# Optimization experiments

Measured on AMD Instinct MI355X. Metric: run time of the kernel, lower is better.

The kernel has to match this reference:

```python
import jax, jax.numpy as jnp
import numpy as np

RES = (128, 128, 128, 100)  # x, y, z, t resolutions
FEAT = 64
N = 1048576
HID = 64
COMBOS4 = [(0, 1), (0, 2), (0, 3), (1, 2), (1, 3), (2, 3)]  # temporal k-planes
COMBOS3 = [(0, 1), (0, 2), (1, 2)]  # spatial triplane


def setup_inputs() -> dict:
    key = jax.random.key(0)
    ks = jax.random.split(key, 16)
    d = {}
    d["inp"] = jax.random.uniform(ks[0], (N, 4), dtype=jnp.float32)  # xyz in [0,1], t in [0,1]
    d["aabb"] = jnp.array([[0.0, 0.0, 0.0], [1.0, 1.0, 1.0]], dtype=jnp.float32)
    # plane coefs: [feat, res[b], res[a]] per combo (a,b), uniform(init_a, init_b)
    for i, (a, b) in enumerate(COMBOS4):
        d[f"tp{i}"] = jax.random.uniform(ks[1 + i], (FEAT, RES[b], RES[a]),
                                         minval=0.1, maxval=0.5, dtype=jnp.float32)
    for i, (a, b) in enumerate(COMBOS3):
        d[f"sp{i}"] = jax.random.uniform(ks[7 + i], (FEAT, RES[b], RES[a]),
                                         minval=0.1, maxval=0.5, dtype=jnp.float32)
    in_dim = 2 * FEAT  # temporal + spatial features concatenated
    d["w0"] = (jax.random.normal(ks[10], (in_dim, HID), dtype=jnp.float32) / np.sqrt(in_dim)).astype(jnp.float32)
    d["b0"] = jnp.zeros((HID,), dtype=jnp.float32)
    d["w1"] = (jax.random.normal(ks[11], (HID, 3), dtype=jnp.float32) / np.sqrt(HID)).astype(jnp.float32)
    d["b1"] = jnp.zeros((3,), dtype=jnp.float32)
    return d


def _sample_plane(plane, cx, cy):
    """Bilinear grid_sample, align_corners=True. plane: [F,H,W]; cx,cy: [N] in [-1,1]. Returns [N,F]."""
    F_, H, W = plane.shape
    x = (cx + 1.0) * 0.5 * (W - 1)
    y = (cy + 1.0) * 0.5 * (H - 1)
    x0 = jnp.clip(jnp.floor(x).astype(jnp.int32), 0, W - 2)
    y0 = jnp.clip(jnp.floor(y).astype(jnp.int32), 0, H - 2)
    wx = (x - x0)[:, None]
    wy = (y - y0)[:, None]
    p = jnp.transpose(plane, (1, 2, 0))  # [H,W,F]
    v00 = p[y0, x0]
    v01 = p[y0, x0 + 1]
    v10 = p[y0 + 1, x0]
    v11 = p[y0 + 1, x0 + 1]
    return (v00 * (1 - wx) + v01 * wx) * (1 - wy) + (v10 * (1 - wx) + v11 * wx) * wy


def reference(inp, aabb, tp0, tp1, tp2, tp3, tp4, tp5, sp0, sp1, sp2, w0, b0, w1, b1):
    # normalize positions to [-1,1]
    pos = (inp[:, :3] - aabb[0]) / (aabb[1] - aabb[0]) * 2.0 - 1.0
    t = inp[:, 3:] * 2.0 - 1.0
    c = jnp.concatenate([pos, t], axis=-1)  # [N,4]
    tps = [tp0, tp1, tp2, tp3, tp4, tp5]
    feat_t = sum(_sample_plane(tps[i], c[:, a], c[:, b]) for i, (a, b) in enumerate(COMBOS4))
    sps = [sp0, sp1, sp2]
    feat_s = sum(_sample_plane(sps[i], pos[:, a], pos[:, b]) for i, (a, b) in enumerate(COMBOS3))
    feat = jnp.concatenate([feat_t, feat_s], axis=-1)  # [N, 2*FEAT]
    h = jax.nn.relu(feat @ w0 + b0)
    return h @ w1 + b1  # [N, 3]
```

## Files before the change

### kernel.cpp

```cpp
#include <hip/hip_runtime.h>
#include <hip/hip_fp16.h>

#define DEVFN __device__ __forceinline__

#if defined(__has_builtin)
#  if __has_builtin(__builtin_amdgcn_fdot2)
#    define HAS_FDOT2 1
#  endif
#endif

typedef _Float16 h2v __attribute__((ext_vector_type(2)));

struct PlanePtrs { const float* p[9]; };

__constant__ const int g_H[9] = {128,128,100,128,100,100,128,128,128};
__constant__ const int g_A[9] = {0,0,0,1,1,2,0,0,1};
__constant__ const int g_B[9] = {1,2,3,2,3,3,1,2,2};
__constant__ const int g_PRE[10] = {0,16384,32768,45568,61952,74752,87552,103936,120320,136704};
__constant__ const int g_OFF4[9] = {0,131072,262144,364544,495616,598016,700416,831488,962560};

static const int    TOTAL_TEXELS = 136704;
static const size_t WS_PLANES    = 17498112ull;
static const size_t WS_W0H       = 16384ull;
static const int    NBINS        = 2048;
static const int    NHB          = 256;

__global__ __launch_bounds__(256) void k_transpose(PlanePtrs ptrs, __half* __restrict__ dst)
{
    int gid = blockIdx.x * 256 + threadIdx.x;

    int pl = 0;
    #pragma unroll
    for (int i = 1; i < 9; ++i) if (gid >= g_PRE[i]) pl = i;
    int tx   = gid - g_PRE[pl];
    int nTex = g_PRE[pl + 1] - g_PRE[pl];

    const float* src = ptrs.p[0];
    #pragma unroll
    for (int i = 1; i < 9; ++i) if (pl == i) src = ptrs.p[i];
    src += tx;

    uint4* __restrict__ out4 = reinterpret_cast<uint4*>(dst) + (size_t)gid * 8;
    #pragma unroll
    for (int j = 0; j < 8; ++j) {
        float f0 = src[(8*j+0)*nTex];
        float f1 = src[(8*j+1)*nTex];
        float f2 = src[(8*j+2)*nTex];
        float f3 = src[(8*j+3)*nTex];
        float f4 = src[(8*j+4)*nTex];
        float f5 = src[(8*j+5)*nTex];
        float f6 = src[(8*j+6)*nTex];
        float f7 = src[(8*j+7)*nTex];
        uint4 u;
        u.x = __builtin_bit_cast(unsigned int, __floats2half2_rn(f0, f1));
        u.y = __builtin_bit_cast(unsigned int, __floats2half2_rn(f2, f3));
        u.z = __builtin_bit_cast(unsigned int, __floats2half2_rn(f4, f5));
        u.w = __builtin_bit_cast(unsigned int, __floats2half2_rn(f6, f7));
        out4[j] = u;
    }
}

__global__ __launch_bounds__(256) void k_w0pack(const float* __restrict__ w0,
                                                unsigned int* __restrict__ w0h)
{
    int idx = blockIdx.x * 256 + threadIdx.x;
    int d = idx >> 6, j = idx & 63;
    float a = w0[(2 * d) * 64 + j];
    float b = w0[(2 * d + 1) * 64 + j];
    w0h[idx] = __builtin_bit_cast(unsigned int, __floats2half2_rn(a, b));
}

DEVFN int point_key(float4 in, float a0x, float a0y, float a0z,
                    float isx, float isy, float isz)
{
    float x = (in.x - a0x) * isx;
    float y = (in.y - a0y) * isy;
    float z = (in.z - a0z) * isz;
    int xc = min(7, max(0, (int)(x * 8.0f)));
    int yc = min(7, max(0, (int)(y * 8.0f)));
    int zc = min(7, max(0, (int)(z * 8.0f)));
    int tc = min(3, max(0, (int)(in.w * 4.0f)));
    return (((xc << 3) | yc) << 3 | zc) << 2 | tc;
}

__global__ __launch_bounds__(256) void k_hist2(const float4* __restrict__ inp,
                                               const float* __restrict__ aabb,
                                               int N, int chunk,
                                               int* __restrict__ blkhist)
{
    __shared__ int hc[NBINS];
    const int tid = threadIdx.x, blk = blockIdx.x;
    #pragma unroll
    for (int j = 0; j < NBINS / 256; ++j) hc[tid + j * 256] = 0;
    __syncthreads();

    float a0x = aabb[0], a0y = aabb[1], a0z = aabb[2];
    float isx = 1.0f / (aabb[3] - a0x), isy = 1.0f / (aabb[4] - a0y), isz = 1.0f / (aabb[5] - a0z);

    int end = min(N, (blk + 1) * chunk);
    for (int i = blk * chunk + tid; i < end; i += 256)
        atomicAdd(&hc[point_key(inp[i], a0x, a0y, a0z, isx, isy, isz)], 1);

    __syncthreads();
    #pragma unroll
    for (int j = 0; j < NBINS / 256; ++j)
        blkhist[blk * NBINS + tid + j * 256] = hc[tid + j * 256];
}

__global__ __launch_bounds__(256) void k_scanA(int* __restrict__ blkhist,
                                               int* __restrict__ bintotal)
{
    int bin = blockIdx.x * 256 + threadIdx.x;
    int run = 0;
    for (int b = 0; b < NHB; ++b) {
        int v = blkhist[b * NBINS + bin];
        blkhist[b * NBINS + bin] = run;
        run += v;
    }
    bintotal[bin] = run;
}

__global__ __launch_bounds__(256) void k_scanB(const int* __restrict__ bintotal,
                                               int* __restrict__ binstart)
{
    int t = threadIdx.x;
    int v[8]; int sum = 0;
    #pragma unroll
    for (int j = 0; j < 8; ++j) { v[j] = bintotal[t * 8 + j]; sum += v[j]; }

    int lane = t & 63, w = t >> 6;
    int x = sum;
    #pragma unroll
    for (int d = 1; d < 64; d <<= 1) {
        int y = __shfl_up(x, d);
        if (lane >= d) x += y;
    }
    __shared__ int wsum[4];
    if (lane == 63) wsum[w] = x;
    __syncthreads();
    int woff = 0;
    for (int i = 0; i < w; ++i) woff += wsum[i];
    int run = woff + x - sum;
    #pragma unroll
    for (int j = 0; j < 8; ++j) { binstart[t * 8 + j] = run; run += v[j]; }
}

__global__ __launch_bounds__(256) void k_fill2(const float4* __restrict__ inp,
                                               const float* __restrict__ aabb,
                                               int N, int chunk,
                                               const int* __restrict__ blkhist,
                                               const int* __restrict__ binstart,
                                               int* __restrict__ order)
{
    __shared__ int hc[NBINS];
    const int tid = threadIdx.x, blk = blockIdx.x;
    #pragma unroll
    for (int j = 0; j < NBINS / 256; ++j) hc[tid + j * 256] = 0;
    __syncthreads();

    float a0x = aabb[0], a0y = aabb[1], a0z = aabb[2];
    float isx = 1.0f / (aabb[3] - a0x), isy = 1.0f / (aabb[4] - a0y), isz = 1.0f / (aabb[5] - a0z);

    int end = min(N, (blk + 1) * chunk);
    for (int i = blk * chunk + tid; i < end; i += 256) {
        int key = point_key(inp[i], a0x, a0y, a0z, isx, isy, isz);
        int lr  = atomicAdd(&hc[key], 1);
        order[binstart[key] + blkhist[blk * NBINS + key] + lr] = i;
    }
}

DEVFN void corner4f(unsigned a, unsigned b, unsigned c, unsigned d,
                    __half2 w00, __half2 w01, __half2 w10, __half2 w11,
                    float& ax, float& ay)
{
    __half2 t = __hmul2(__builtin_bit_cast(__half2, a), w00);
    t = __hfma2(__builtin_bit_cast(__half2, b), w01, t);
    t = __hfma2(__builtin_bit_cast(__half2, c), w10, t);
    t = __hfma2(__builtin_bit_cast(__half2, d), w11, t);
    ax += __low2float(t);
    ay += __high2float(t);
}

__global__ __launch_bounds__(64) void k_main(
    const float4* __restrict__ inp,
    const float*  __restrict__ aabb,
    const __half* __restrict__ planes,
    const unsigned int* __restrict__ w0h,
    const int*    __restrict__ order,
    int           useOrder,
    const float*  __restrict__ w0,
    const float*  __restrict__ b0,
    const float*  __restrict__ w1,
    const float*  __restrict__ b1,
    float*        __restrict__ out)
{
    __shared__ unsigned int lds[64 * 65];

    const int tid = threadIdx.x;
    const int g   = tid >> 3;
    const int k   = tid & 7;

    const int nwg = gridDim.x;
    const int bid = blockIdx.x;
    const int wid = ((nwg & 7) == 0) ? ((bid & 7) * (nwg >> 3) + (bid >> 3)) : bid;
    const int base = wid * 64;

    const int myord = useOrder ? order[base + tid] : (base + tid);

    float a0x = aabb[0], a0y = aabb[1], a0z = aabb[2];
    float sx  = aabb[3] - a0x, sy = aabb[4] - a0y, sz = aabb[5] - a0z;

    for (int q = 0; q < 8; ++q) {
        const int p = g * 8 + q;
        const int pidx = __shfl(myord, p);
        float4 in = inp[pidx];
        float c[4];
        c[0] = (in.x - a0x) / sx * 2.0f - 1.0f;
        c[1] = (in.y - a0y) / sy * 2.0f - 1.0f;
        c[2] = (in.z - a0z) / sz * 2.0f - 1.0f;
        c[3] = in.w * 2.0f - 1.0f;

        float accT[8], accS[8];
        #pragma unroll
        for (int j = 0; j < 8; ++j) { accT[j] = 0.0f; accS[j] = 0.0f; }

        #pragma unroll
        for (int pl = 0; pl < 9; ++pl) {
            const int W = 128;
            const int H = g_H[pl];
            float fx = (c[g_A[pl]] + 1.0f) * 0.5f * (float)(W - 1);
            float fy = (c[g_B[pl]] + 1.0f) * 0.5f * (float)(H - 1);
            int x0 = min(max((int)floorf(fx), 0), W - 2);
            int y0 = min(max((int)floorf(fy), 0), H - 2);
            float wx = fx - (float)x0;
            float wy = fy - (float)y0;
            float iwx = 1.0f - wx, iwy = 1.0f - wy;

            const uint4* pb = reinterpret_cast<const uint4*>(planes)
                            + g_OFF4[pl] + ((y0 << 7) + x0) * 8 + k;
            uint4 v00 = pb[0];
            uint4 v01 = pb[8];
            uint4 v10 = pb[1024];
            uint4 v11 = pb[1032];

            __half2 w00h = __float2half2_rn(iwx * iwy);
            __half2 w01h = __float2half2_rn(wx  * iwy);
            __half2 w10h = __float2half2_rn(iwx * wy);
            __half2 w11h = __float2half2_rn(wx  * wy);

            if (pl < 6) {
                corner4f(v00.x, v01.x, v10.x, v11.x, w00h, w01h, w10h, w11h, accT[0], accT[1]);
                corner4f(v00.y, v01.y, v10.y, v11.y, w00h, w01h, w10h, w11h, accT[2], accT[3]);
                corner4f(v00.z, v01.z, v10.z, v11.z, w00h, w01h, w10h, w11h, accT[4], accT[5]);
                corner4f(v00.w, v01.w, v10.w, v11.w, w00h, w01h, w10h, w11h, accT[6], accT[7]);
            } else {
                corner4f(v00.x, v01.x, v10.x, v11.x, w00h, w01h, w10h, w11h, accS[0], accS[1]);
                corner4f(v00.y, v01.y, v10.y, v11.y, w00h, w01h, w10h, w11h, accS[2], accS[3]);
                corner4f(v00.z, v01.z, v10.z, v11.z, w00h, w01h, w10h, w11h, accS[4], accS[5]);
                corner4f(v00.w, v01.w, v10.w, v11.w, w00h, w01h, w10h, w11h, accS[6], accS[7]);
            }
        }

        #pragma unroll
        for (int j = 0; j < 4; ++j) {
            lds[p * 65 +      k * 4 + j] =
                __builtin_bit_cast(unsigned int, __floats2half2_rn(accT[2*j], accT[2*j+1]));
            lds[p * 65 + 32 + k * 4 + j] =
                __builtin_bit_cast(unsigned int, __floats2half2_rn(accS[2*j], accS[2*j+1]));
        }
    }

    __syncthreads();

    const unsigned int* lrow = &lds[tid * 65];
    float o0 = b1[0], o1 = b1[1], o2 = b1[2];

    #pragma unroll 1
    for (int jc = 0; jc < 64; jc += 16) {
        float h[16];
        #pragma unroll
        for (int jj = 0; jj < 16; ++jj) h[jj] = b0[jc + jj];

        #pragma unroll 4
        for (int d = 0; d < 64; ++d) {
            unsigned u = lrow[d];
#if defined(HAS_FDOT2)
            h2v fv = __builtin_bit_cast(h2v, u);
            const unsigned int* wr = w0h + d * 64 + jc;
            #pragma unroll
            for (int jj = 0; jj < 16; ++jj)
                h[jj] = __builtin_amdgcn_fdot2(fv, __builtin_bit_cast(h2v, wr[jj]),
                                               h[jj], false);
#else
            __half2 hv = __builtin_bit_cast(__half2, u);
            float f0 = __low2float(hv);
            float f1 = __high2float(hv);
            const float* wr = w0 + d * 128 + jc;
            #pragma unroll
            for (int jj = 0; jj < 16; ++jj) h[jj] = fmaf(f0, wr[jj], h[jj]);
            #pragma unroll
            for (int jj = 0; jj < 16; ++jj) h[jj] = fmaf(f1, wr[64 + jj], h[jj]);
#endif
        }

        #pragma unroll
        for (int jj = 0; jj < 16; ++jj) {
            float r = fmaxf(h[jj], 0.0f);
            const float* wq = w1 + (jc + jj) * 3;
            o0 = fmaf(r, wq[0], o0);
            o1 = fmaf(r, wq[1], o1);
            o2 = fmaf(r, wq[2], o2);
        }
    }

    long long oo = (long long)myord * 3;
    out[oo + 0] = o0;
    out[oo + 1] = o1;
    out[oo + 2] = o2;
}

__global__ __launch_bounds__(256) void k_fallback(
    const float4* __restrict__ inp, const float* __restrict__ aabb, PlanePtrs ptrs,
    const float* __restrict__ w0, const float* __restrict__ b0,
    const float* __restrict__ w1, const float* __restrict__ b1,
    float* __restrict__ out, int N, int start)
{
    int pidx = start + blockIdx.x * 256 + threadIdx.x;
    if (pidx >= N) return;
    float4 in = inp[pidx];
    float c[4];
    c[0] = (in.x - aabb[0]) / (aabb[3] - aabb[0]) * 2.0f - 1.0f;
    c[1] = (in.y - aabb[1]) / (aabb[4] - aabb[1]) * 2.0f - 1.0f;
    c[2] = (in.z - aabb[2]) / (aabb[5] - aabb[2]) * 2.0f - 1.0f;
    c[3] = in.w * 2.0f - 1.0f;

    float h[64];
    #pragma unroll
    for (int j = 0; j < 64; ++j) h[j] = b0[j];

    #pragma unroll
    for (int pl = 0; pl < 9; ++pl) {
        const int W = 128, H = g_H[pl];
        float fx = (c[g_A[pl]] + 1.0f) * 0.5f * (float)(W - 1);
        float fy = (c[g_B[pl]] + 1.0f) * 0.5f * (float)(H - 1);
        int x0 = min(max((int)floorf(fx), 0), W - 2);
        int y0 = min(max((int)floorf(fy), 0), H - 2);
        float wx = fx - (float)x0, wy = fy - (float)y0;
        const float* P = ptrs.p[pl];
        int off = y0 * 128 + x0;
        int HW = H * 128;
        int row = (pl < 6) ? 0 : 64;
        for (int f = 0; f < 64; ++f) {
            const float* qp = P + f * HW + off;
            float v = (qp[0] * (1.0f - wx) + qp[1] * wx) * (1.0f - wy)
                    + (qp[128] * (1.0f - wx) + qp[129] * wx) * wy;
            const float* wr = w0 + (row + f) * 64;
            #pragma unroll
            for (int j = 0; j < 64; ++j) h[j] = fmaf(v, wr[j], h[j]);
        }
    }
    float o0 = b1[0], o1 = b1[1], o2 = b1[2];
    #pragma unroll
    for (int j = 0; j < 64; ++j) {
        float r = fmaxf(h[j], 0.0f);
        o0 = fmaf(r, w1[j * 3 + 0], o0);
        o1 = fmaf(r, w1[j * 3 + 1], o1);
        o2 = fmaf(r, w1[j * 3 + 2], o2);
    }
    out[(long long)pidx * 3 + 0] = o0;
    out[(long long)pidx * 3 + 1] = o1;
    out[(long long)pidx * 3 + 2] = o2;
}

extern "C" void kernel_launch(void* const* d_in, const int* in_sizes, int n_in,
                              void* d_out, int out_size, void* d_ws, size_t ws_size,
                              hipStream_t stream)
{
    const float4* inp  = (const float4*)d_in[0];
    const float*  aabb = (const float*)d_in[1];
    PlanePtrs ptrs;
    for (int i = 0; i < 9; ++i) ptrs.p[i] = (const float*)d_in[2 + i];
    const float* w0 = (const float*)d_in[11];
    const float* b0 = (const float*)d_in[12];
    const float* w1 = (const float*)d_in[13];
    const float* b1 = (const float*)d_in[14];
    float* out = (float*)d_out;
    const int N = in_sizes[0] / 4;

    const size_t off_w0h   = WS_PLANES;
    const size_t ws_base   = WS_PLANES + WS_W0H;
    const size_t off_order = ws_base;
    const size_t off_bh    = off_order + 4ull * (size_t)N;
    const size_t off_bt    = off_bh + (size_t)NHB * NBINS * 4;
    const size_t off_bs    = off_bt + NBINS * 4;
    const size_t need_sort = off_bs + NBINS * 4;

    if (ws_size >= ws_base && (N % 64) == 0) {
        __half* planes = (__half*)d_ws;
        unsigned int* w0h = (unsigned int*)((char*)d_ws + off_w0h);
        k_transpose<<<TOTAL_TEXELS / 256, 256, 0, stream>>>(ptrs, planes);
        k_w0pack<<<16, 256, 0, stream>>>(w0, w0h);

        if (ws_size >= need_sort) {
            int* order    = (int*)((char*)d_ws + off_order);
            int* blkhist  = (int*)((char*)d_ws + off_bh);
            int* bintotal = (int*)((char*)d_ws + off_bt);
            int* binstart = (int*)((char*)d_ws + off_bs);
            int chunk = (((N + NHB - 1) / NHB) + 255) / 256 * 256;

            k_hist2<<<NHB, 256, 0, stream>>>(inp, aabb, N, chunk, blkhist);
            k_scanA<<<NBINS / 256, 256, 0, stream>>>(blkhist, bintotal);
            k_scanB<<<1, 256, 0, stream>>>(bintotal, binstart);
            k_fill2<<<NHB, 256, 0, stream>>>(inp, aabb, N, chunk, blkhist, binstart, order);
            k_main<<<N / 64, 64, 0, stream>>>(inp, aabb, planes, w0h, order, 1,
                                              w0, b0, w1, b1, out);
        } else {
            k_main<<<N / 64, 64, 0, stream>>>(inp, aabb, planes, w0h, (const int*)nullptr, 0,
                                              w0, b0, w1, b1, out);
        }
    } else {
        k_fallback<<<(N + 255) / 256, 256, 0, stream>>>(inp, aabb, ptrs, w0, b0, w1, b1, out, N, 0);
    }
}
```

Baseline: 363.5 us.

## Software-pipeline plane gathers with 4-deep register ring and shuffle coords

Each lane now loads and normalizes its own input point once, and the coordinates are broadcast with shuffles instead of every lane re-reading inp through a shuffled index. All 9 plane offsets and bilinear weights are computed up front. Corner loads run through a 4-slot register ring so that up to four planes' gathers are in flight while earlier planes are accumulated. The outer q loop is marked unroll 1. This raises register pressure (64 VGPRs for the ring plus the weights) and may cut occupancy.

```diff
diff --git a/kernel.cpp b/kernel.cpp
--- a/kernel.cpp
+++ b/kernel.cpp
@@ -210,54 +210,85 @@
     float a0x = aabb[0], a0y = aabb[1], a0z = aabb[2];
     float sx  = aabb[3] - a0x, sy = aabb[4] - a0y, sz = aabb[5] - a0z;
 
+    float4 min_ = inp[myord];
+    float c0 = (min_.x - a0x) / sx * 2.0f - 1.0f;
+    float c1 = (min_.y - a0y) / sy * 2.0f - 1.0f;
+    float c2 = (min_.z - a0z) / sz * 2.0f - 1.0f;
+    float c3 = min_.w * 2.0f - 1.0f;
+
+    const uint4* pbase = reinterpret_cast<const uint4*>(planes);
+
+    #pragma unroll 1
     for (int q = 0; q < 8; ++q) {
         const int p = g * 8 + q;
-        const int pidx = __shfl(myord, p);
-        float4 in = inp[pidx];
-        float c[4];
-        c[0] = (in.x - a0x) / sx * 2.0f - 1.0f;
-        c[1] = (in.y - a0y) / sy * 2.0f - 1.0f;
-        c[2] = (in.z - a0z) / sz * 2.0f - 1.0f;
-        c[3] = in.w * 2.0f - 1.0f;
-
-        float accT[8], accS[8];
-        #pragma unroll
-        for (int j = 0; j < 8; ++j) { accT[j] = 0.0f; accS[j] = 0.0f; }
-
+        float cc[4];
+        cc[0] = __shfl(c0, p);
+        cc[1] = __shfl(c1, p);
+        cc[2] = __shfl(c2, p);
+        cc[3] = __shfl(c3, p);
+
+        int     offv[9];
+        __half2 Wv[9][4];
         #pragma unroll
         for (int pl = 0; pl < 9; ++pl) {
             const int W = 128;
             const int H = g_H[pl];
-            float fx = (c[g_A[pl]] + 1.0f) * 0.5f * (float)(W - 1);
-            float fy = (c[g_B[pl]] + 1.0f) * 0.5f * (float)(H - 1);
+            float fx = (cc[g_A[pl]] + 1.0f) * 0.5f * (float)(W - 1);
+            float fy = (cc[g_B[pl]] + 1.0f) * 0.5f * (float)(H - 1);
             int x0 = min(max((int)floorf(fx), 0), W - 2);
             int y0 = min(max((int)floorf(fy), 0), H - 2);
             float wx = fx - (float)x0;
             float wy = fy - (float)y0;
             float iwx = 1.0f - wx, iwy = 1.0f - wy;
-
-            const uint4* pb = reinterpret_cast<const uint4*>(planes)
-                            + g_OFF4[pl] + ((y0 << 7) + x0) * 8 + k;
-            uint4 v00 = pb[0];
-            uint4 v01 = pb[8];
-            uint4 v10 = pb[1024];
-            uint4 v11 = pb[1032];
-
-            __half2 w00h = __float2half2_rn(iwx * iwy);
-            __half2 w01h = __float2half2_rn(wx  * iwy);
-            __half2 w10h = __float2half2_rn(iwx * wy);
-            __half2 w11h = __float2half2_rn(wx  * wy);
-
+            offv[pl]  = g_OFF4[pl] + ((y0 << 7) + x0) * 8 + k;
+            Wv[pl][0] = __float2half2_rn(iwx * iwy);
+            Wv[pl][1] = __float2half2_rn(wx  * iwy);
+            Wv[pl][2] = __float2half2_rn(iwx * wy);
+            Wv[pl][3] = __float2half2_rn(wx  * wy);
+        }
+
+        uint4 v00[4], v01[4], v10[4], v11[4];
+        #pragma unroll
+        for (int s = 0; s < 4; ++s) {
+            const uint4* pb = pbase + offv[s];
+            v00[s] = pb[0];
+            v01[s] = pb[8];
+            v10[s] = pb[1024];
+            v11[s] = pb[1032];
+        }
+
+        float accT[8], accS[8];
+        #pragma unroll
+        for (int j = 0; j < 8; ++j) { accT[j] = 0.0f; accS[j] = 0.0f; }
+
+        #pragma unroll
+        for (int pl = 0; pl < 9; ++pl) {
+            const int s = pl & 3;
             if (pl < 6) {
-                corner4f(v00.x, v01.x, v10.x, v11.x, w00h, w01h, w10h, w11h, accT[0], accT[1]);
-                corner4f(v00.y, v01.y, v10.y, v11.y, w00h, w01h, w10h, w11h, accT[2], accT[3]);
-                corner4f(v00.z, v01.z, v10.z, v11.z, w00h, w01h, w10h, w11h, accT[4], accT[5]);
-                corner4f(v00.w, v01.w, v10.w, v11.w, w00h, w01h, w10h, w11h, accT[6], accT[7]);
+                corner4f(v00[s].x, v01[s].x, v10[s].x, v11[s].x,
+                         Wv[pl][0], Wv[pl][1], Wv[pl][2], Wv[pl][3], accT[0], accT[1]);
+                corner4f(v00[s].y, v01[s].y, v10[s].y, v11[s].y,
+                         Wv[pl][0], Wv[pl][1], Wv[pl][2], Wv[pl][3], accT[2], accT[3]);
+                corner4f(v00[s].z, v01[s].z, v10[s].z, v11[s].z,
+                         Wv[pl][0], Wv[pl][1], Wv[pl][2], Wv[pl][3], accT[4], accT[5]);
+                corner4f(v00[s].w, v01[s].w, v10[s].w, v11[s].w,
+                         Wv[pl][0], Wv[pl][1], Wv[pl][2], Wv[pl][3], accT[6], accT[7]);
             } else {
-                corner4f(v00.x, v01.x, v10.x, v11.x, w00h, w01h, w10h, w11h, accS[0], accS[1]);
-                corner4f(v00.y, v01.y, v10.y, v11.y, w00h, w01h, w10h, w11h, accS[2], accS[3]);
-                corner4f(v00.z, v01.z, v10.z, v11.z, w00h, w01h, w10h, w11h, accS[4], accS[5]);
-                corner4f(v00.w, v01.w, v10.w, v11.w, w00h, w01h, w10h, w11h, accS[6], accS[7]);
+                corner4f(v00[s].x, v01[s].x, v10[s].x, v11[s].x,
+                         Wv[pl][0], Wv[pl][1], Wv[pl][2], Wv[pl][3], accS[0], accS[1]);
+                corner4f(v00[s].y, v01[s].y, v10[s].y, v11[s].y,
+                         Wv[pl][0], Wv[pl][1], Wv[pl][2], Wv[pl][3], accS[2], accS[3]);
+                corner4f(v00[s].z, v01[s].z, v10[s].z, v11[s].z,
+                         Wv[pl][0], Wv[pl][1], Wv[pl][2], Wv[pl][3], accS[4], accS[5]);
+                corner4f(v00[s].w, v01[s].w, v10[s].w, v11[s].w,
+                         Wv[pl][0], Wv[pl][1], Wv[pl][2], Wv[pl][3], accS[6], accS[7]);
+            }
+            if (pl + 4 < 9) {
+                const uint4* pb = pbase + offv[pl + 4];
+                v00[s] = pb[0];
+                v01[s] = pb[8];
+                v10[s] = pb[1024];
+                v11[s] = pb[1032];
             }
         }
 
```

Measured after the change: 348.9 us (median of 2 runs). 4.0% less time.
